# Performance work log

Measured on AMD Instinct MI355X. Metric: run time of the kernel, lower is better.

## Reference

```python
import jax, jax.numpy as jnp
import numpy as np

N, B, H, NH = 16384, 64, 256, 8
MAXN = 512
EPS = 1e-5


def setup_inputs() -> dict:
    key = jax.random.key(0)
    ks = jax.random.split(key, 8)
    s = 0.02
    return {
        "x": jax.random.normal(ks[0], (N, H), jnp.float32),
        "batch": jnp.sort(jax.random.randint(ks[1], (N,), 0, B)),
        "max_nodes": MAXN,
        "norm1_w": jnp.ones((H,), jnp.float32),
        "norm1_b": jnp.zeros((H,), jnp.float32),
        "in_proj_w": jax.random.normal(ks[2], (3 * H, H), jnp.float32) * s,
        "in_proj_b": jnp.zeros((3 * H,), jnp.float32),
        "out_proj_w": jax.random.normal(ks[3], (H, H), jnp.float32) * s,
        "out_proj_b": jnp.zeros((H,), jnp.float32),
        "norm2_w": jnp.ones((H,), jnp.float32),
        "norm2_b": jnp.zeros((H,), jnp.float32),
        "ffn_w1": jax.random.normal(ks[4], (4 * H, H), jnp.float32) * s,
        "ffn_b1": jnp.zeros((4 * H,), jnp.float32),
        "ffn_w2": jax.random.normal(ks[5], (H, 4 * H), jnp.float32) * s,
        "ffn_b2": jnp.zeros((H,), jnp.float32),
    }


def _graph_norm(x, batch, countsf, w, b):
    # Per-graph mean and unbiased std (torch.std default), eps added to std.
    mean = jax.ops.segment_sum(x, batch, num_segments=B) / countsf[:, None]
    c = x - mean[batch]
    var = jax.ops.segment_sum(c * c, batch, num_segments=B) / jnp.maximum(countsf - 1.0, 1.0)[:, None]
    std = jnp.sqrt(var) + EPS
    return w * (c / std[batch]) + b


def _forward(x, batch, max_nodes, norm1_w, norm1_b, in_proj_w, in_proj_b,
             out_proj_w, out_proj_b, norm2_w, norm2_b, ffn_w1, ffn_b1, ffn_w2, ffn_b2):
    n = x.shape[0]
    counts = jax.ops.segment_sum(jnp.ones((n,), jnp.int32), batch, num_segments=B)  # [B]
    countsf = counts.astype(x.dtype)
    starts = jnp.concatenate([jnp.zeros((1,), jnp.int32), jnp.cumsum(counts)[:-1]])
    pos = jnp.arange(n, dtype=jnp.int32) - starts[batch]  # position within graph (batch is sorted)

    # GraphNorm 1, then pack ragged -> padded [B, M, H]
    xn = _graph_norm(x, batch, countsf, norm1_w, norm1_b)
    x_pad = jnp.zeros((B, max_nodes, H), x.dtype).at[batch, pos].set(xn)
    key_valid = jnp.arange(max_nodes)[None, :] < counts[:, None]  # [B, M] True=real node

    # Multi-head attention (eval mode, key_padding_mask)
    qkv = x_pad @ in_proj_w.T + in_proj_b  # [B, M, 3H]
    q, k, v = jnp.split(qkv, 3, axis=-1)
    hd = H // NH
    heads = lambda t: t.reshape(B, max_nodes, NH, hd).transpose(0, 2, 1, 3)  # [B, NH, M, hd]
    q, k, v = heads(q), heads(k), heads(v)
    scores = jnp.einsum('bhqd,bhkd->bhqk', q, k) / np.float32(np.sqrt(hd))
    scores = jnp.where(key_valid[:, None, None, :], scores, jnp.float32(-1e9))
    attn = jax.nn.softmax(scores, axis=-1)
    ctx = jnp.einsum('bhqk,bhkd->bhqd', attn, v).transpose(0, 2, 1, 3).reshape(B, max_nodes, H)
    attn_out = ctx @ out_proj_w.T + out_proj_b

    # Unpack padded -> ragged, residual
    x = x + attn_out[batch, pos]

    # GraphNorm 2 + FFN (exact GELU) + residual
    xn2 = _graph_norm(x, batch, countsf, norm2_w, norm2_b)
    h = jax.nn.gelu(xn2 @ ffn_w1.T + ffn_b1, approximate=False)
    return x + (h @ ffn_w2.T + ffn_b2)


def reference(x, batch, max_nodes, norm1_w, norm1_b, in_proj_w, in_proj_b,
              out_proj_w, out_proj_b, norm2_w, norm2_b, ffn_w1, ffn_b1, ffn_w2, ffn_b2):
    return _forward(x, batch, max_nodes, norm1_w, norm1_b, in_proj_w, in_proj_b,
                    out_proj_w, out_proj_b, norm2_w, norm2_b, ffn_w1, ffn_b1, ffn_w2, ffn_b2)
```

## Files before the change

### kernel.cpp

```cpp
#include <hip/hip_runtime.h>
#include <hip/hip_bf16.h>
#include <math.h>

typedef __bf16 bf16;
typedef bf16 bf16x4 __attribute__((ext_vector_type(4)));
typedef bf16 bf16x8 __attribute__((ext_vector_type(8)));
typedef float f32x4 __attribute__((ext_vector_type(4)));

#define NNODES 16384
#define NB 64
#define HDIM 256
#define NHEADS 8
#define HD 32
#define GN_STRIPS 16

typedef __attribute__((address_space(3))) unsigned int lds_u32;
typedef __attribute__((address_space(1))) const unsigned int glb_u32;

__device__ __forceinline__ void async_copy16(const bf16* gsrc, bf16* ldst) {
    __builtin_amdgcn_global_load_lds((glb_u32*)gsrc, (lds_u32*)ldst, 16, 0, 0);
}

__global__ void cvt_all(const float* __restrict__ pw_q, const float* __restrict__ pw_o,
                        const float* __restrict__ pw_1, const float* __restrict__ pw_2,
                        bf16* __restrict__ dq, bf16* __restrict__ d_o,
                        bf16* __restrict__ d1, bf16* __restrict__ d2,
                        const int* __restrict__ batch, int* __restrict__ starts,
                        int* __restrict__ counts) {
    if (blockIdx.x == 0 && threadIdx.x < 64) {
        int b = threadIdx.x;
        int lo = 0, hi = NNODES;
        while (lo < hi) { int mid = (lo + hi) >> 1; if (batch[mid] < b) lo = mid + 1; else hi = mid; }
        int s0 = lo;
        lo = 0; hi = NNODES;
        while (lo < hi) { int mid = (lo + hi) >> 1; if (batch[mid] < b + 1) lo = mid + 1; else hi = mid; }
        starts[b] = s0;
        counts[b] = lo - s0;
    }
    int i = blockIdx.x * 256 + threadIdx.x;
    const float* src; bf16* dst; int j;
    if (i < 49152)       { src = pw_q; dst = dq;  j = i; }
    else if (i < 65536)  { src = pw_o; dst = d_o; j = i - 49152; }
    else if (i < 131072) { src = pw_1; dst = d1;  j = i - 65536; }
    else                 { src = pw_2; dst = d2;  j = i - 131072; }
    float4 v = *(const float4*)(src + (size_t)j * 4);
    bf16x4 o;
    o[0] = (bf16)v.x; o[1] = (bf16)v.y; o[2] = (bf16)v.z; o[3] = (bf16)v.w;
    *(bf16x4*)(dst + (size_t)j * 4) = o;
}

__global__ __launch_bounds__(256) void gn_partial(
    const float* __restrict__ x, const int* __restrict__ starts,
    const int* __restrict__ counts, float* __restrict__ part) {
    int g = blockIdx.x, strip = blockIdx.y, hh = threadIdx.x;
    int s = starts[g], c = counts[g];
    int chunk = (c + GN_STRIPS - 1) / GN_STRIPS;
    int r0 = strip * chunk, r1 = min(c, r0 + chunk);
    float sum = 0.f, sq = 0.f;
    for (int r = r0; r < r1; ++r) {
        float v = x[(size_t)(s + r) * HDIM + hh];
        sum += v; sq += v * v;
    }
    part[((size_t)(g * GN_STRIPS + strip) * 2 + 0) * HDIM + hh] = sum;
    part[((size_t)(g * GN_STRIPS + strip) * 2 + 1) * HDIM + hh] = sq;
}

__global__ __launch_bounds__(256) void gn_final(
    const float* __restrict__ part, const int* __restrict__ counts,
    const float* __restrict__ w, const float* __restrict__ b, float* __restrict__ stats) {
    int g = blockIdx.x, hh = threadIdx.x;
    float sum = 0.f, sq = 0.f;
    for (int st = 0; st < GN_STRIPS; ++st) {
        sum += part[((size_t)(g * GN_STRIPS + st) * 2 + 0) * HDIM + hh];
        sq  += part[((size_t)(g * GN_STRIPS + st) * 2 + 1) * HDIM + hh];
    }
    float cf = (float)counts[g];
    float mean = sum / cf;
    float var = (sq - cf * mean * mean) / fmaxf(cf - 1.f, 1.f);
    var = fmaxf(var, 0.f);
    float inv = 1.f / (sqrtf(var) + 1e-5f);
    float a = w[hh] * inv;
    stats[(size_t)g * 512 + hh] = a;
    stats[(size_t)g * 512 + 256 + hh] = b[hh] - mean * a;
}

__global__ __launch_bounds__(256) void gn_apply(
    const float* __restrict__ x, const int* __restrict__ batch,
    const float* __restrict__ stats, bf16* __restrict__ out) {
    size_t i = ((size_t)blockIdx.x * 256 + threadIdx.x) * 4;
    int row = (int)(i >> 8);
    int g = batch[row];
    int hh = (int)(i & 255);
    float4 xv = *(const float4*)(x + i);
    float4 av = *(const float4*)(stats + (size_t)g * 512 + hh);
    float4 bv = *(const float4*)(stats + (size_t)g * 512 + 256 + hh);
    bf16x4 o;
    o[0] = (bf16)(av.x * xv.x + bv.x);
    o[1] = (bf16)(av.y * xv.y + bv.y);
    o[2] = (bf16)(av.z * xv.z + bv.z);
    o[3] = (bf16)(av.w * xv.w + bv.w);
    *(bf16x4*)(out + i) = o;
}

template <int MODE>
__global__ __launch_bounds__(256) void gemm_tn64(
    const bf16* __restrict__ A, const bf16* __restrict__ B,
    const float* __restrict__ bias, void* __restrict__ Cout,
    int M, int N, int K) {
    __shared__ __align__(16) bf16 As[64 * 32];
    __shared__ __align__(16) bf16 Bs[128 * 32];
    const int row0 = blockIdx.x * 64;
    const int col0 = blockIdx.y * 128;
    const int tid = threadIdx.x;
    const int lane = tid & 63;
    const int wave = tid >> 6;
    const int wn = wave * 32;
    const int lr = lane & 15;
    const int lk = lane >> 4;
    const int ra = tid >> 2, oa = (tid & 3) * 8;

    const bf16* Ab = A + (size_t)row0 * K;
    const bf16* Bb = B + (size_t)col0 * K;

    f32x4 acc[4][2] = {};

    for (int k0 = 0; k0 < K; k0 += 32) {
        __syncthreads();
        async_copy16(Ab + (size_t)ra * K + k0 + oa, &As[tid * 8]);
        async_copy16(Bb + (size_t)ra * K + k0 + oa, &Bs[tid * 8]);
        async_copy16(Bb + (size_t)(ra + 64) * K + k0 + oa, &Bs[(tid + 256) * 8]);
        __syncthreads();
        bf16x8 af[4], bfr[2];
#pragma unroll
        for (int mi = 0; mi < 4; ++mi)
            af[mi] = *(const bf16x8*)&As[(mi * 16 + lr) * 32 + lk * 8];
#pragma unroll
        for (int ni = 0; ni < 2; ++ni)
            bfr[ni] = *(const bf16x8*)&Bs[(wn + ni * 16 + lr) * 32 + lk * 8];
#pragma unroll
        for (int mi = 0; mi < 4; ++mi)
#pragma unroll
            for (int ni = 0; ni < 2; ++ni)
                acc[mi][ni] = __builtin_amdgcn_mfma_f32_16x16x32_bf16(af[mi], bfr[ni], acc[mi][ni], 0, 0, 0);
    }

#pragma unroll
    for (int mi = 0; mi < 4; ++mi) {
#pragma unroll
        for (int ni = 0; ni < 2; ++ni) {
            const int col = col0 + wn + ni * 16 + lr;
            const float bv = bias[col];
#pragma unroll
            for (int r = 0; r < 4; ++r) {
                const int row = row0 + mi * 16 + lk * 4 + r;
                float v = acc[mi][ni][r] + bv;
                size_t idx = (size_t)row * N + col;
                if (MODE == 0) {
                    ((bf16*)Cout)[idx] = (bf16)v;
                } else {
                    float gel = 0.5f * v * (1.f + erff(v * 0.70710678118654752f));
                    ((bf16*)Cout)[idx] = (bf16)gel;
                }
            }
        }
    }
}

__global__ __launch_bounds__(256) void gemm_small_res(
    const bf16* __restrict__ A, const bf16* __restrict__ B,
    const float* __restrict__ bias, const float* __restrict__ res,
    float* __restrict__ Cout, int M, int N, int K) {
    __shared__ __align__(16) bf16 As[64 * 32];
    __shared__ __align__(16) bf16 Bs[64 * 32];
    const int row0 = blockIdx.x * 64;
    const int col0 = blockIdx.y * 64;
    const int tid = threadIdx.x;
    const int lane = tid & 63;
    const int wave = tid >> 6;
    const int wr = (wave >> 1) * 32;
    const int wc = (wave & 1) * 32;
    const int lr = lane & 15;
    const int lk = lane >> 4;
    const int rs = tid >> 2, os = (tid & 3) * 8;

    const bf16* Ab = A + (size_t)row0 * K;
    const bf16* Bb = B + (size_t)col0 * K;

    f32x4 acc[2][2] = {};

    for (int k0 = 0; k0 < K; k0 += 32) {
        __syncthreads();
        async_copy16(Ab + (size_t)rs * K + k0 + os, &As[tid * 8]);
        async_copy16(Bb + (size_t)rs * K + k0 + os, &Bs[tid * 8]);
        __syncthreads();
        bf16x8 af[2], bfr[2];
#pragma unroll
        for (int mi = 0; mi < 2; ++mi)
            af[mi] = *(const bf16x8*)&As[(wr + mi * 16 + lr) * 32 + lk * 8];
#pragma unroll
        for (int ni = 0; ni < 2; ++ni)
            bfr[ni] = *(const bf16x8*)&Bs[(wc + ni * 16 + lr) * 32 + lk * 8];
#pragma unroll
        for (int mi = 0; mi < 2; ++mi)
#pragma unroll
            for (int ni = 0; ni < 2; ++ni)
                acc[mi][ni] = __builtin_amdgcn_mfma_f32_16x16x32_bf16(af[mi], bfr[ni], acc[mi][ni], 0, 0, 0);
    }

#pragma unroll
    for (int mi = 0; mi < 2; ++mi) {
#pragma unroll
        for (int ni = 0; ni < 2; ++ni) {
            const int col = col0 + wc + ni * 16 + lr;
            const float bv = bias[col];
#pragma unroll
            for (int r = 0; r < 4; ++r) {
                const int row = row0 + wr + mi * 16 + lk * 4 + r;
                size_t idx = (size_t)row * N + col;
                Cout[idx] = acc[mi][ni][r] + bv + res[idx];
            }
        }
    }
}

__global__ __launch_bounds__(256) void attn_mfma(
    const bf16* __restrict__ qkv, const int* __restrict__ starts,
    const int* __restrict__ counts, bf16* __restrict__ ctx) {
    int g = blockIdx.x, h = blockIdx.y, qc = blockIdx.z;
    int s = starts[g], c = counts[g];
    if (qc * 256 >= c) return;
    __shared__ __align__(16) bf16 Qs[256][40];
    __shared__ __align__(16) bf16 Ks[64][40];
    __shared__ __align__(16) bf16 Vt[32][72];
    __shared__ __align__(16) bf16 Ps[4][64][72];
    __shared__ float Ls[4][64];
    const int tid = threadIdx.x;
    const int w = tid >> 6, lane = tid & 63;
    const int lo = lane & 15, hi = lane >> 4;
    const float scale = 0.17677669529663687f;
    const int nkt = (c + 63) >> 6;

    {
        int qrow = qc * 256 + tid;
        const bf16* qp = qkv + (size_t)(s + qrow) * 768 + h * HD;
#pragma unroll
        for (int t4 = 0; t4 < 4; ++t4) {
            bf16x8 sv;
            if (qrow < c) {
                bf16x8 v = *(const bf16x8*)(qp + t4 * 8);
#pragma unroll
                for (int u = 0; u < 8; ++u) sv[u] = (bf16)((float)v[u] * scale);
            } else {
#pragma unroll
                for (int u = 0; u < 8; ++u) sv[u] = (bf16)0.f;
            }
            *(bf16x8*)&Qs[tid][t4 * 8] = sv;
        }
    }
    __syncthreads();
    bf16x8 bq[4];
#pragma unroll
    for (int nt = 0; nt < 4; ++nt) bq[nt] = *(const bf16x8*)&Qs[w * 64 + nt * 16 + lo][hi * 8];

    f32x4 ctxa[4][2] = {};
    float l[4] = {0.f, 0.f, 0.f, 0.f};

    for (int kt = 0; kt < nkt; ++kt) {
        {
            int krow = kt * 64 + (tid >> 2);
            bf16x8 v;
            if (krow < c) v = *(const bf16x8*)(qkv + (size_t)(s + krow) * 768 + 256 + h * HD + (tid & 3) * 8);
            else {
#pragma unroll
                for (int u = 0; u < 8; ++u) v[u] = (bf16)0.f;
            }
            *(bf16x8*)&Ks[tid >> 2][(tid & 3) * 8] = v;
        }
        {
            int vrow = kt * 64 + (tid & 63);
            int dg = tid >> 6;
            bf16x8 v;
            if (vrow < c) v = *(const bf16x8*)(qkv + (size_t)(s + vrow) * 768 + 512 + h * HD + dg * 8);
            else {
#pragma unroll
                for (int u = 0; u < 8; ++u) v[u] = (bf16)0.f;
            }
#pragma unroll
            for (int u = 0; u < 8; ++u) Vt[dg * 8 + u][tid & 63] = v[u];
        }
        __syncthreads();

        f32x4 sacc[4][4] = {};
#pragma unroll
        for (int kmt = 0; kmt < 4; ++kmt) {
            bf16x8 ak = *(const bf16x8*)&Ks[kmt * 16 + lo][hi * 8];
#pragma unroll
            for (int nt = 0; nt < 4; ++nt)
                sacc[kmt][nt] = __builtin_amdgcn_mfma_f32_16x16x32_bf16(ak, bq[nt], sacc[kmt][nt], 0, 0, 0);
        }
#pragma unroll
        for (int kmt = 0; kmt < 4; ++kmt) {
            int kbase = kt * 64 + kmt * 16 + hi * 4;
#pragma unroll
            for (int nt = 0; nt < 4; ++nt) {
                bf16x4 pv;
#pragma unroll
                for (int r = 0; r < 4; ++r) {
                    float p = (kbase + r < c) ? __expf(sacc[kmt][nt][r]) : 0.f;
                    l[nt] += p;
                    pv[r] = (bf16)p;
                }
                *(bf16x4*)&Ps[w][nt * 16 + lo][kmt * 16 + hi * 4] = pv;
            }
        }
#pragma unroll
        for (int ks = 0; ks < 2; ++ks) {
            bf16x8 bv[2];
#pragma unroll
            for (int dn = 0; dn < 2; ++dn) bv[dn] = *(const bf16x8*)&Vt[dn * 16 + lo][ks * 32 + hi * 8];
#pragma unroll
            for (int qmt = 0; qmt < 4; ++qmt) {
                bf16x8 ap = *(const bf16x8*)&Ps[w][qmt * 16 + lo][ks * 32 + hi * 8];
#pragma unroll
                for (int dn = 0; dn < 2; ++dn)
                    ctxa[qmt][dn] = __builtin_amdgcn_mfma_f32_16x16x32_bf16(ap, bv[dn], ctxa[qmt][dn], 0, 0, 0);
            }
        }
        __syncthreads();
    }

#pragma unroll
    for (int nt = 0; nt < 4; ++nt) {
        l[nt] += __shfl_xor(l[nt], 16);
        l[nt] += __shfl_xor(l[nt], 32);
    }
    if (hi == 0) {
#pragma unroll
        for (int nt = 0; nt < 4; ++nt) Ls[w][nt * 16 + lo] = l[nt];
    }
#pragma unroll
    for (int qmt = 0; qmt < 4; ++qmt) {
#pragma unroll
        for (int r = 0; r < 4; ++r) {
            int qrow = qc * 256 + w * 64 + qmt * 16 + hi * 4 + r;
            if (qrow < c) {
                float linv = 1.f / Ls[w][qmt * 16 + hi * 4 + r];
                bf16* op = ctx + (size_t)(s + qrow) * HDIM + h * HD;
#pragma unroll
                for (int dn = 0; dn < 2; ++dn)
                    op[dn * 16 + lo] = (bf16)(ctxa[qmt][dn][r] * linv);
            }
        }
    }
}

extern "C" void kernel_launch(void* const* d_in, const int* in_sizes, int n_in,
                              void* d_out, int out_size, void* d_ws, size_t ws_size,
                              hipStream_t stream) {
    const float* x        = (const float*)d_in[0];
    const int*   batch    = (const int*)d_in[1];
    const float* norm1_w  = (const float*)d_in[3];
    const float* norm1_b  = (const float*)d_in[4];
    const float* in_proj_w  = (const float*)d_in[5];
    const float* in_proj_b  = (const float*)d_in[6];
    const float* out_proj_w = (const float*)d_in[7];
    const float* out_proj_b = (const float*)d_in[8];
    const float* norm2_w  = (const float*)d_in[9];
    const float* norm2_b  = (const float*)d_in[10];
    const float* ffn_w1   = (const float*)d_in[11];
    const float* ffn_b1   = (const float*)d_in[12];
    const float* ffn_w2   = (const float*)d_in[13];
    const float* ffn_b2   = (const float*)d_in[14];
    float* out = (float*)d_out;

    char* ws = (char*)d_ws;
    size_t off = 0;
    auto alloc = [&](size_t bytes) -> void* {
        void* p = ws + off;
        off += bytes;
        off = (off + 255) & ~(size_t)255;
        return p;
    };
    int*  starts = (int*)alloc(NB * 4);
    int*  counts = (int*)alloc(NB * 4);
    bf16* wq = (bf16*)alloc((size_t)768 * 256 * 2);
    bf16* wo = (bf16*)alloc((size_t)256 * 256 * 2);
    bf16* w1 = (bf16*)alloc((size_t)1024 * 256 * 2);
    bf16* w2 = (bf16*)alloc((size_t)256 * 1024 * 2);
    bf16* t0  = (bf16*)alloc((size_t)NNODES * HDIM * 2);
    bf16* qkv = (bf16*)alloc((size_t)NNODES * 768 * 2);
    float* y  = (float*)alloc((size_t)NNODES * HDIM * 4);
    bf16* hbuf = (bf16*)alloc((size_t)NNODES * 1024 * 2);
    float* gnpart = (float*)alloc((size_t)NB * GN_STRIPS * 2 * HDIM * 4);
    float* gnstats = (float*)alloc((size_t)NB * 512 * 4);

    cvt_all<<<196608 / 256, 256, 0, stream>>>(in_proj_w, out_proj_w, ffn_w1, ffn_w2,
                                              wq, wo, w1, w2, batch, starts, counts);
    gn_partial<<<dim3(NB, GN_STRIPS), 256, 0, stream>>>(x, starts, counts, gnpart);
    gn_final<<<NB, 256, 0, stream>>>(gnpart, counts, norm1_w, norm1_b, gnstats);
    gn_apply<<<NNODES * HDIM / 1024, 256, 0, stream>>>(x, batch, gnstats, t0);
    gemm_tn64<0><<<dim3(NNODES / 64, 768 / 128), 256, 0, stream>>>(
        t0, wq, in_proj_b, qkv, NNODES, 768, 256);
    attn_mfma<<<dim3(NB, NHEADS, 2), 256, 0, stream>>>(qkv, starts, counts, t0);
    gemm_small_res<<<dim3(NNODES / 64, 256 / 64), 256, 0, stream>>>(
        t0, wo, out_proj_b, x, y, NNODES, 256, 256);
    gn_partial<<<dim3(NB, GN_STRIPS), 256, 0, stream>>>(y, starts, counts, gnpart);
    gn_final<<<NB, 256, 0, stream>>>(gnpart, counts, norm2_w, norm2_b, gnstats);
    gn_apply<<<NNODES * HDIM / 1024, 256, 0, stream>>>(y, batch, gnstats, t0);
    gemm_tn64<2><<<dim3(NNODES / 64, 1024 / 128), 256, 0, stream>>>(
        t0, w1, ffn_b1, hbuf, NNODES, 1024, 256);
    gemm_small_res<<<dim3(NNODES / 64, 256 / 64), 256, 0, stream>>>(
        hbuf, w2, ffn_b2, y, out, NNODES, 256, 1024);
}
```

Baseline: 230.9 us.

## Fold GraphNorm finalize into atomics and add small-tail attention path

```diff
diff --git a/kernel.cpp b/kernel.cpp
--- a/kernel.cpp
+++ b/kernel.cpp
@@ -26,16 +26,24 @@
                         bf16* __restrict__ dq, bf16* __restrict__ d_o,
                         bf16* __restrict__ d1, bf16* __restrict__ d2,
                         const int* __restrict__ batch, int* __restrict__ starts,
-                        int* __restrict__ counts) {
-    if (blockIdx.x == 0 && threadIdx.x < 64) {
-        int b = threadIdx.x;
-        int lo = 0, hi = NNODES;
-        while (lo < hi) { int mid = (lo + hi) >> 1; if (batch[mid] < b) lo = mid + 1; else hi = mid; }
-        int s0 = lo;
-        lo = 0; hi = NNODES;
-        while (lo < hi) { int mid = (lo + hi) >> 1; if (batch[mid] < b + 1) lo = mid + 1; else hi = mid; }
-        starts[b] = s0;
-        counts[b] = lo - s0;
+                        int* __restrict__ counts, float* __restrict__ gstats) {
+    if (blockIdx.x >= 768) {
+        int zb = blockIdx.x - 768;
+        float4 z = {0.f, 0.f, 0.f, 0.f};
+        float4* p = (float4*)gstats + (size_t)zb * 2048 + threadIdx.x;
+#pragma unroll
+        for (int j = 0; j < 8; ++j) p[j * 256] = z;
+        if (blockIdx.x == 768 && threadIdx.x < 64) {
+            int b = threadIdx.x;
+            int lo = 0, hi = NNODES;
+            while (lo < hi) { int mid = (lo + hi) >> 1; if (batch[mid] < b) lo = mid + 1; else hi = mid; }
+            int s0 = lo;
+            lo = 0; hi = NNODES;
+            while (lo < hi) { int mid = (lo + hi) >> 1; if (batch[mid] < b + 1) lo = mid + 1; else hi = mid; }
+            starts[b] = s0;
+            counts[b] = lo - s0;
+        }
+        return;
     }
     int i = blockIdx.x * 256 + threadIdx.x;
     const float* src; bf16* dst; int j;
@@ -51,7 +59,7 @@
 
 __global__ __launch_bounds__(256) void gn_partial(
     const float* __restrict__ x, const int* __restrict__ starts,
-    const int* __restrict__ counts, float* __restrict__ part) {
+    const int* __restrict__ counts, float* __restrict__ gsum, float* __restrict__ gsq) {
     int g = blockIdx.x, strip = blockIdx.y, hh = threadIdx.x;
     int s = starts[g], c = counts[g];
     int chunk = (c + GN_STRIPS - 1) / GN_STRIPS;
@@ -61,44 +69,42 @@
         float v = x[(size_t)(s + r) * HDIM + hh];
         sum += v; sq += v * v;
     }
-    part[((size_t)(g * GN_STRIPS + strip) * 2 + 0) * HDIM + hh] = sum;
-    part[((size_t)(g * GN_STRIPS + strip) * 2 + 1) * HDIM + hh] = sq;
-}
-
-__global__ __launch_bounds__(256) void gn_final(
-    const float* __restrict__ part, const int* __restrict__ counts,
-    const float* __restrict__ w, const float* __restrict__ b, float* __restrict__ stats) {
-    int g = blockIdx.x, hh = threadIdx.x;
-    float sum = 0.f, sq = 0.f;
-    for (int st = 0; st < GN_STRIPS; ++st) {
-        sum += part[((size_t)(g * GN_STRIPS + st) * 2 + 0) * HDIM + hh];
-        sq  += part[((size_t)(g * GN_STRIPS + st) * 2 + 1) * HDIM + hh];
-    }
-    float cf = (float)counts[g];
-    float mean = sum / cf;
-    float var = (sq - cf * mean * mean) / fmaxf(cf - 1.f, 1.f);
-    var = fmaxf(var, 0.f);
-    float inv = 1.f / (sqrtf(var) + 1e-5f);
-    float a = w[hh] * inv;
-    stats[(size_t)g * 512 + hh] = a;
-    stats[(size_t)g * 512 + 256 + hh] = b[hh] - mean * a;
+    if (r1 > r0) {
+        atomicAdd(&gsum[g * HDIM + hh], sum);
+        atomicAdd(&gsq[g * HDIM + hh], sq);
+    }
 }
 
 __global__ __launch_bounds__(256) void gn_apply(
     const float* __restrict__ x, const int* __restrict__ batch,
-    const float* __restrict__ stats, bf16* __restrict__ out) {
+    const float* __restrict__ gsum, const float* __restrict__ gsq,
+    const int* __restrict__ counts, const float* __restrict__ w,
+    const float* __restrict__ b, bf16* __restrict__ out) {
     size_t i = ((size_t)blockIdx.x * 256 + threadIdx.x) * 4;
     int row = (int)(i >> 8);
     int g = batch[row];
     int hh = (int)(i & 255);
+    float cf = (float)counts[g];
+    float inv_c = 1.f / cf;
+    float inv_c1 = 1.f / fmaxf(cf - 1.f, 1.f);
+    float4 sv = *(const float4*)(gsum + g * HDIM + hh);
+    float4 qv = *(const float4*)(gsq + g * HDIM + hh);
     float4 xv = *(const float4*)(x + i);
-    float4 av = *(const float4*)(stats + (size_t)g * 512 + hh);
-    float4 bv = *(const float4*)(stats + (size_t)g * 512 + 256 + hh);
+    float4 wv = *(const float4*)(w + hh);
+    float4 bv = *(const float4*)(b + hh);
     bf16x4 o;
-    o[0] = (bf16)(av.x * xv.x + bv.x);
-    o[1] = (bf16)(av.y * xv.y + bv.y);
-    o[2] = (bf16)(av.z * xv.z + bv.z);
-    o[3] = (bf16)(av.w * xv.w + bv.w);
+#define GN_ONE(S, Q, X, W, B, IDX)                                          \
+    {                                                                       \
+        float mean = (S) * inv_c;                                           \
+        float var = fmaxf(((Q) - cf * mean * mean) * inv_c1, 0.f);          \
+        float a = (W) / (sqrtf(var) + 1e-5f);                               \
+        o[IDX] = (bf16)(a * ((X) - mean) + (B));                            \
+    }
+    GN_ONE(sv.x, qv.x, xv.x, wv.x, bv.x, 0)
+    GN_ONE(sv.y, qv.y, xv.y, wv.y, bv.y, 1)
+    GN_ONE(sv.z, qv.z, xv.z, wv.z, bv.z, 2)
+    GN_ONE(sv.w, qv.w, xv.w, wv.w, bv.w, 3)
+#undef GN_ONE
     *(bf16x4*)(out + i) = o;
 }
 
@@ -239,6 +245,125 @@
     const int lo = lane & 15, hi = lane >> 4;
     const float scale = 0.17677669529663687f;
     const int nkt = (c + 63) >> 6;
+    const int rem = c - qc * 256;
+
+    if (rem <= 64) {
+        {
+            int qr = (tid >> 2);
+            int qrow = qc * 256 + qr;
+            bf16x8 sv;
+            if (qrow < c) {
+                bf16x8 v = *(const bf16x8*)(qkv + (size_t)(s + qrow) * 768 + h * HD + (tid & 3) * 8);
+#pragma unroll
+                for (int u = 0; u < 8; ++u) sv[u] = (bf16)((float)v[u] * scale);
+            } else {
+#pragma unroll
+                for (int u = 0; u < 8; ++u) sv[u] = (bf16)0.f;
+            }
+            *(bf16x8*)&Qs[qr][(tid & 3) * 8] = sv;
+        }
+        __syncthreads();
+        bf16x8 bq[4];
+#pragma unroll
+        for (int nt = 0; nt < 4; ++nt) bq[nt] = *(const bf16x8*)&Qs[nt * 16 + lo][hi * 8];
+
+        f32x4 ctxa[4][2] = {};
+        float l[4] = {0.f, 0.f, 0.f, 0.f};
+
+        for (int kt = w; kt < nkt; kt += 4) {
+            f32x4 sacc[4][4] = {};
+#pragma unroll
+            for (int kmt = 0; kmt < 4; ++kmt) {
+                int krow = kt * 64 + kmt * 16 + lo;
+                bf16x8 ak;
+                if (krow < c) ak = *(const bf16x8*)(qkv + (size_t)(s + krow) * 768 + 256 + h * HD + hi * 8);
+                else {
+#pragma unroll
+                    for (int u = 0; u < 8; ++u) ak[u] = (bf16)0.f;
+                }
+#pragma unroll
+                for (int nt = 0; nt < 4; ++nt)
+                    sacc[kmt][nt] = __builtin_amdgcn_mfma_f32_16x16x32_bf16(ak, bq[nt], sacc[kmt][nt], 0, 0, 0);
+            }
+#pragma unroll
+            for (int kmt = 0; kmt < 4; ++kmt) {
+                int kbase = kt * 64 + kmt * 16 + hi * 4;
+#pragma unroll
+                for (int nt = 0; nt < 4; ++nt) {
+                    bf16x4 pv;
+#pragma unroll
+                    for (int r = 0; r < 4; ++r) {
+                        float p = (kbase + r < c) ? __expf(sacc[kmt][nt][r]) : 0.f;
+                        l[nt] += p;
+                        pv[r] = (bf16)p;
+                    }
+                    *(bf16x4*)&Ps[w][nt * 16 + lo][kmt * 16 + hi * 4] = pv;
+                }
+            }
+#pragma unroll
+            for (int ks = 0; ks < 2; ++ks) {
+                bf16x8 bv[2];
+#pragma unroll
+                for (int dn = 0; dn < 2; ++dn) {
+#pragma unroll
+                    for (int u = 0; u < 8; ++u) {
+                        int vrow = kt * 64 + ks * 32 + hi * 8 + u;
+                        bv[dn][u] = (vrow < c)
+                            ? qkv[(size_t)(s + vrow) * 768 + 512 + h * HD + dn * 16 + lo]
+                            : (bf16)0.f;
+                    }
+                }
+#pragma unroll
+                for (int qmt = 0; qmt < 4; ++qmt) {
+                    bf16x8 ap = *(const bf16x8*)&Ps[w][qmt * 16 + lo][ks * 32 + hi * 8];
+#pragma unroll
+                    for (int dn = 0; dn < 2; ++dn)
+                        ctxa[qmt][dn] = __builtin_amdgcn_mfma_f32_16x16x32_bf16(ap, bv[dn], ctxa[qmt][dn], 0, 0, 0);
+                }
+            }
+        }
+
+#pragma unroll
+        for (int nt = 0; nt < 4; ++nt) {
+            l[nt] += __shfl_xor(l[nt], 16);
+            l[nt] += __shfl_xor(l[nt], 32);
+        }
+        if (hi == 0) {
+#pragma unroll
+            for (int nt = 0; nt < 4; ++nt) Ls[w][nt * 16 + lo] = l[nt];
+        }
+        float* Fw = (float*)&Ps[w][0][0];
+        __syncthreads();
+#pragma unroll
+        for (int qmt = 0; qmt < 4; ++qmt)
+#pragma unroll
+            for (int dn = 0; dn < 2; ++dn)
+#pragma unroll
+                for (int r = 0; r < 4; ++r)
+                    Fw[(qmt * 16 + hi * 4 + r) * 32 + dn * 16 + lo] = ctxa[qmt][dn][r];
+        __syncthreads();
+        {
+            int qr = tid >> 2;
+            int qrow = qc * 256 + qr;
+            if (qrow < c) {
+                int d0 = (tid & 3) * 8;
+                float lsum = Ls[0][qr] + Ls[1][qr] + Ls[2][qr] + Ls[3][qr];
+                float linv = 1.f / lsum;
+                const float* F0 = (const float*)&Ps[0][0][0];
+                const float* F1 = (const float*)&Ps[1][0][0];
+                const float* F2 = (const float*)&Ps[2][0][0];
+                const float* F3 = (const float*)&Ps[3][0][0];
+                bf16x8 o;
+#pragma unroll
+                for (int j = 0; j < 8; ++j) {
+                    int idx = qr * 32 + d0 + j;
+                    o[j] = (bf16)((F0[idx] + F1[idx] + F2[idx] + F3[idx]) * linv);
+                }
+                *(bf16x8*)(ctx + (size_t)(s + qrow) * HDIM + h * HD + d0) = o;
+            }
+        }
+        return;
+    }
 
     {
         int qrow = qc * 256 + tid;
@@ -391,22 +516,25 @@
     bf16* qkv = (bf16*)alloc((size_t)NNODES * 768 * 2);
     float* y  = (float*)alloc((size_t)NNODES * HDIM * 4);
     bf16* hbuf = (bf16*)alloc((size_t)NNODES * 1024 * 2);
-    float* gnpart = (float*)alloc((size_t)NB * GN_STRIPS * 2 * HDIM * 4);
-    float* gnstats = (float*)alloc((size_t)NB * 512 * 4);
-
-    cvt_all<<<196608 / 256, 256, 0, stream>>>(in_proj_w, out_proj_w, ffn_w1, ffn_w2,
-                                              wq, wo, w1, w2, batch, starts, counts);
-    gn_partial<<<dim3(NB, GN_STRIPS), 256, 0, stream>>>(x, starts, counts, gnpart);
-    gn_final<<<NB, 256, 0, stream>>>(gnpart, counts, norm1_w, norm1_b, gnstats);
-    gn_apply<<<NNODES * HDIM / 1024, 256, 0, stream>>>(x, batch, gnstats, t0);
+    float* gstats = (float*)alloc((size_t)4 * NB * HDIM * 4);
+    float* gsum1 = gstats;
+    float* gsq1  = gstats + NB * HDIM;
+    float* gsum2 = gstats + 2 * NB * HDIM;
+    float* gsq2  = gstats + 3 * NB * HDIM;
+
+    cvt_all<<<776, 256, 0, stream>>>(in_proj_w, out_proj_w, ffn_w1, ffn_w2,
+                                     wq, wo, w1, w2, batch, starts, counts, gstats);
+    gn_partial<<<dim3(NB, GN_STRIPS), 256, 0, stream>>>(x, starts, counts, gsum1, gsq1);
+    gn_apply<<<NNODES * HDIM / 1024, 256, 0, stream>>>(x, batch, gsum1, gsq1, counts,
+                                                       norm1_w, norm1_b, t0);
     gemm_tn64<0><<<dim3(NNODES / 64, 768 / 128), 256, 0, stream>>>(
         t0, wq, in_proj_b, qkv, NNODES, 768, 256);
     attn_mfma<<<dim3(NB, NHEADS, 2), 256, 0, stream>>>(qkv, starts, counts, t0);
     gemm_small_res<<<dim3(NNODES / 64, 256 / 64), 256, 0, stream>>>(
         t0, wo, out_proj_b, x, y, NNODES, 256, 256);
-    gn_partial<<<dim3(NB, GN_STRIPS), 256, 0, stream>>>(y, starts, counts, gnpart);
-    gn_final<<<NB, 256, 0, stream>>>(gnpart, counts, norm2_w, norm2_b, gnstats);
-    gn_apply<<<NNODES * HDIM / 1024, 256, 0, stream>>>(y, batch, gnstats, t0);
+    gn_partial<<<dim3(NB, GN_STRIPS), 256, 0, stream>>>(y, starts, counts, gsum2, gsq2);
+    gn_apply<<<NNODES * HDIM / 1024, 256, 0, stream>>>(y, batch, gsum2, gsq2, counts,
+                                                       norm2_w, norm2_b, t0);
     gemm_tn64<2><<<dim3(NNODES / 64, 1024 / 128), 256, 0, stream>>>(
         t0, w1, ffn_b1, hbuf, NNODES, 1024, 256);
     gemm_small_res<<<dim3(NNODES / 64, 256 / 64), 256, 0, stream>>>(
```

Result: faster. 222.9 us (-3.5%).
